# Kernel tuning notes

Measured on AMD Instinct MI355X. Metric: run time of the kernel, lower is better.

## Reference

```python
import jax, jax.numpy as jnp
import numpy as np

EPS = 1e-6

def _ln(x, g, b):
    mu = jnp.mean(x, axis=-1, keepdims=True)
    var = jnp.mean(jnp.square(x - mu), axis=-1, keepdims=True)
    return (x - mu) * jax.lax.rsqrt(var + EPS) * g + b

def setup_inputs() -> dict:
    key = jax.random.key(0)
    ks = jax.random.split(key, 8)
    B, T, D = 4, 4096, 1024
    H = 16
    Dff = 4 * D
    s = 1.0 / np.sqrt(D)
    sf = 1.0 / np.sqrt(Dff)
    return {
        "x": jax.random.normal(ks[0], (B, T, D), dtype=jnp.float32),
        "wq": jax.random.uniform(ks[1], (D, D), jnp.float32, -s, s),
        "wk": jax.random.uniform(ks[2], (D, D), jnp.float32, -s, s),
        "wv": jax.random.uniform(ks[3], (D, D), jnp.float32, -s, s),
        "wo": jax.random.uniform(ks[4], (D, D), jnp.float32, -s, s),
        "ln1_g": jnp.ones((D,), jnp.float32),
        "ln1_b": jnp.zeros((D,), jnp.float32),
        "w1": jax.random.uniform(ks[5], (D, Dff), jnp.float32, -s, s),
        "b1": jnp.zeros((Dff,), jnp.float32),
        "w2": jax.random.uniform(ks[6], (Dff, D), jnp.float32, -sf, sf),
        "b2": jnp.zeros((D,), jnp.float32),
        "ln2_g": jnp.ones((D,), jnp.float32),
        "ln2_b": jnp.zeros((D,), jnp.float32),
    }

def reference(x, wq, wk, wv, wo, ln1_g, ln1_b, w1, b1, w2, b2, ln2_g, ln2_b):
    B, T, D = x.shape
    H = 16
    dk = D // H
    x1 = _ln(x, ln1_g, ln1_b)
    q = (x1 @ wq).reshape(B, T, H, dk)
    k = (x1 @ wk).reshape(B, T, H, dk)
    v = (x1 @ wv).reshape(B, T, H, dk)
    # NOTE: faithful to source -- attention mixes HEADS at each token position
    # attn[b,t,h,g] = softmax_g( sum_d q[b,t,h,d]*k[b,t,g,d] / sqrt(dk) )
    attn = jax.nn.softmax(jnp.einsum('bthd,btgd->bthg', q / np.sqrt(dk), k), axis=-1)
    o = jnp.einsum('bthg,btgd->bthd', attn, v)
    # faithful head-major reshape: transpose(1,2).contiguous().view(B,T,-1)
    o = jnp.transpose(o, (0, 2, 1, 3)).reshape(B, T, H * dk)
    o = o @ wo
    q2 = _ln(o + x, ln1_g, ln1_b)  # same layer_norm params reused
    h = jax.nn.gelu(q2 @ w1 + b1, approximate=False)
    y = h @ w2 + b2 + q2
    return _ln(y, ln2_g, ln2_b)
```

## Files before the change

### kernel.cpp

```cpp
#include <hip/hip_runtime.h>


typedef __attribute__((ext_vector_type(8))) short s16x8;
typedef __attribute__((ext_vector_type(4))) short s16x4;
typedef __attribute__((ext_vector_type(4))) float f32x4;

__device__ __forceinline__ short f2bf(float x) {
  unsigned u = __builtin_bit_cast(unsigned, x);
  u = (u + 0x7FFFu + ((u >> 16) & 1u)) >> 16;
  return (short)u;
}
__device__ __forceinline__ float bf2f(short s) {
  unsigned u = ((unsigned)(unsigned short)s) << 16;
  return __builtin_bit_cast(float, u);
}

__device__ __forceinline__ void ld_g2l16(const short* g, const short* l) {
  __builtin_amdgcn_global_load_lds(
      (const __attribute__((address_space(1))) void*)g,
      (__attribute__((address_space(3))) void*)l, 16, 0, 0);
}

__device__ __forceinline__ s16x8 lds_read8(const short* smem, int off) {
  const __attribute__((address_space(3))) short* p =
      (const __attribute__((address_space(3))) short*)smem;
  return *(const __attribute__((address_space(3))) s16x8*)(p + off);
}
__device__ __forceinline__ void lds_wr_f32(const short* smem, int foff,
                                           float v) {
  __attribute__((address_space(3))) float* p =
      (__attribute__((address_space(3))) float*)smem;
  p[foff] = v;
}
__device__ __forceinline__ float lds_rd_f32(const short* smem, int foff) {
  const __attribute__((address_space(3))) float* p =
      (const __attribute__((address_space(3))) float*)smem;
  return p[foff];
}

__device__ __forceinline__ float fast_gelu(float v) {
  float y = 0.7978845608f * (v + 0.044715f * v * v * v);
  float ay = fabsf(y);
  float t = __expf(-2.0f * ay);
  float th = (1.0f - t) * __frcp_rn(1.0f + t);
  th = (y >= 0.f) ? th : -th;
  return 0.5f * v * (1.0f + th);
}

#define MFMA16(va, vb, vc) \
  __builtin_amdgcn_mfma_f32_16x16x32_bf16(va, vb, vc, 0, 0, 0)

template <int EPI>
__device__ __forceinline__ void epi_chunk(
    const short* smem, int two, int lane, const f32x4* accm ,
    void* __restrict__ outp, const float* __restrict__ bias, int N, int rowb,
    int nb) {
  const int cc16 = lane & 15, hq = lane >> 4;
#pragma unroll
  for (int n = 0; n < 4; ++n)
#pragma unroll
    for (int r = 0; r < 4; ++r)
      lds_wr_f32(smem, two + (n * 16 + cc16) * 17 + hq * 4 + r, accm[n][r]);
  asm volatile("s_waitcnt lgkmcnt(0)" ::: "memory");
  if constexpr (EPI == 0 || EPI == 2) {
    const int grp = lane & 7;
#pragma unroll
    for (int p = 0; p < 2; ++p) {
      const int row = p * 8 + (lane >> 3);
      const int colb = grp * 8;
      s16x8 ov;
#pragma unroll
      for (int i = 0; i < 8; ++i) {
        float v = lds_rd_f32(smem, two + (colb + i) * 17 + row);
        if constexpr (EPI == 2) v = fast_gelu(v + bias[nb + colb + i]);
        ov[i] = f2bf(v);
      }
      *(s16x8*)((short*)outp + (size_t)(rowb + row) * N + nb + colb) = ov;
    }
  } else {
    const int seg = lane & 3;
    const int row = lane >> 2;
#pragma unroll
    for (int k = 0; k < 4; ++k) {
      const int colb = seg * 4 + k * 16;
      float4 v4;
      v4.x = lds_rd_f32(smem, two + (colb + 0) * 17 + row);
      v4.y = lds_rd_f32(smem, two + (colb + 1) * 17 + row);
      v4.z = lds_rd_f32(smem, two + (colb + 2) * 17 + row);
      v4.w = lds_rd_f32(smem, two + (colb + 3) * 17 + row);
      float* gp = (float*)outp + (size_t)(rowb + row) * N + nb + colb;
      if constexpr (EPI == 4) {
        float4 pv = *(const float4*)gp;
        v4.x += pv.x; v4.y += pv.y; v4.z += pv.z; v4.w += pv.w;
        if (bias) {
          v4.x += bias[nb + colb + 0];
          v4.y += bias[nb + colb + 1];
          v4.z += bias[nb + colb + 2];
          v4.w += bias[nb + colb + 3];
        }
      }
      *(float4*)gp = v4;
    }
  }
  asm volatile("s_waitcnt lgkmcnt(0)" ::: "memory");
}

template <int EPI>
__global__ __launch_bounds__(512, 2) void gemm256(
    const short* __restrict__ A, const short* __restrict__ BT,
    void* __restrict__ outp, const float* __restrict__ bias, int N, int K) {
  extern __shared__ __align__(16) short smem[];

  const int t = threadIdx.x;
  const int lane = t & 63, w = t >> 6;
  const int wm = w >> 2, wn = w & 3;

  const int nbn = N >> 8;
  const int oi = (int)blockIdx.x;
  const int seq = oi >> 3;
  const int bq = seq / nbn;
  const int bm = (oi & 7) * 8 + bq;
  const int bn = seq - bq * nbn;

  const int l8 = lane >> 3;
  const int lcw = ((lane & 7) ^ l8) * 8;
  const short* gA = A + (size_t)(bm * 256 + w * 8 + l8) * K + lcw;
  const short* gB = BT + (size_t)(bn * 256 + w * 8 + l8) * K + lcw;
  const int lb = w * 512;

  auto stage = [&](const short* g, int bufo, int h, int kt) {
    const int go = h * 128 * K + kt * 64;
    ld_g2l16(g + go, smem + bufo + h * 8192 + lb);
    ld_g2l16(g + go + 64 * K, smem + bufo + h * 8192 + 4096 + lb);
  };

  const int fr = lane & 15, fc = lane >> 4;
  const int baseA = (wm * 128 + fr) * 64;
  const int baseB = (wn * 64 + fr) * 64;
  const int sl0 = (fc ^ (fr & 7)) * 8;
  const int sl1 = ((4 + fc) ^ (fr & 7)) * 8;

  f32x4 acc[8][4];
#pragma unroll
  for (int m = 0; m < 8; ++m)
#pragma unroll
    for (int n = 0; n < 4; ++n) acc[m][n] = (f32x4){0.f, 0.f, 0.f, 0.f};

  const int nt = K >> 6;

  stage(gA, 0, 0, 0);
  stage(gA, 0, 1, 0);
  stage(gB, 32768, 0, 0);
  stage(gB, 32768, 1, 0);
  if (nt > 1) {
    stage(gA, 16384, 0, 1);
    stage(gA, 16384, 1, 1);
    stage(gB, 49152, 0, 1);
    stage(gB, 49152, 1, 1);
    asm volatile("s_waitcnt vmcnt(8)" ::: "memory");
  } else {
    asm volatile("s_waitcnt vmcnt(0)" ::: "memory");
  }
  __builtin_amdgcn_s_barrier();
  asm volatile("" ::: "memory");

  for (int u = 0; u < nt; ++u) {
    const bool pf = (u + 2 < nt);
    const int pa = (u & 1) << 14;
    const int pb = 32768 + pa;

    s16x8 a0[4][2], a1[4][2], b0[2][2], b1[2][2];
#pragma unroll
    for (int mi = 0; mi < 4; ++mi) {
      a0[mi][0] = lds_read8(smem, pa + baseA + mi * 1024 + sl0);
      a0[mi][1] = lds_read8(smem, pa + baseA + mi * 1024 + sl1);
    }
#pragma unroll
    for (int ni = 0; ni < 2; ++ni) {
      b0[ni][0] = lds_read8(smem, pb + baseB + ni * 1024 + sl0);
      b0[ni][1] = lds_read8(smem, pb + baseB + ni * 1024 + sl1);
    }
#pragma unroll
    for (int ni = 0; ni < 2; ++ni) {
      b1[ni][0] = lds_read8(smem, pb + baseB + 2048 + ni * 1024 + sl0);
      b1[ni][1] = lds_read8(smem, pb + baseB + 2048 + ni * 1024 + sl1);
    }
#pragma unroll
    for (int mi = 0; mi < 4; ++mi) {
      a1[mi][0] = lds_read8(smem, pa + baseA + 4096 + mi * 1024 + sl0);
      a1[mi][1] = lds_read8(smem, pa + baseA + 4096 + mi * 1024 + sl1);
    }

    __builtin_amdgcn_s_setprio(1);
#pragma unroll
    for (int mi = 0; mi < 4; ++mi)
#pragma unroll
      for (int ni = 0; ni < 2; ++ni) {
        acc[mi][ni] = MFMA16(a0[mi][0], b0[ni][0], acc[mi][ni]);
        acc[mi][ni] = MFMA16(a0[mi][1], b0[ni][1], acc[mi][ni]);
      }
#pragma unroll
    for (int mi = 0; mi < 4; ++mi)
#pragma unroll
      for (int ni = 0; ni < 2; ++ni) {
        acc[mi][2 + ni] = MFMA16(a0[mi][0], b1[ni][0], acc[mi][2 + ni]);
        acc[mi][2 + ni] = MFMA16(a0[mi][1], b1[ni][1], acc[mi][2 + ni]);
      }
#pragma unroll
    for (int mi = 0; mi < 4; ++mi)
#pragma unroll
      for (int ni = 0; ni < 2; ++ni) {
        acc[4 + mi][2 + ni] = MFMA16(a1[mi][0], b1[ni][0], acc[4 + mi][2 + ni]);
        acc[4 + mi][2 + ni] = MFMA16(a1[mi][1], b1[ni][1], acc[4 + mi][2 + ni]);
      }
    __builtin_amdgcn_s_setprio(0);

    asm volatile("s_waitcnt lgkmcnt(0)" ::: "memory");
    __builtin_amdgcn_s_barrier();
    asm volatile("" ::: "memory");

    if (pf) {
      stage(gB, pb, 0, u + 2);
      stage(gB, pb, 1, u + 2);
      stage(gA, pa, 0, u + 2);
      stage(gA, pa, 1, u + 2);
    }

    __builtin_amdgcn_s_setprio(1);
#pragma unroll
    for (int mi = 0; mi < 4; ++mi)
#pragma unroll
      for (int ni = 0; ni < 2; ++ni) {
        acc[4 + mi][ni] = MFMA16(a1[mi][0], b0[ni][0], acc[4 + mi][ni]);
        acc[4 + mi][ni] = MFMA16(a1[mi][1], b0[ni][1], acc[4 + mi][ni]);
      }
    __builtin_amdgcn_s_setprio(0);

    if (pf) {
      asm volatile("s_waitcnt vmcnt(8)" ::: "memory");
    } else {
      asm volatile("s_waitcnt vmcnt(0)" ::: "memory");
    }
    __builtin_amdgcn_s_barrier();
    asm volatile("" ::: "memory");
  }

  const int two = w * 1088;
  const int mb = bm * 256 + wm * 128;
  const int nb = bn * 256 + wn * 64;
#pragma unroll
  for (int m = 0; m < 8; ++m)
    epi_chunk<EPI>(smem, two, lane, acc[m], outp, bias, N, mb + m * 16, nb);
}

template <int EPI>
__global__ __launch_bounds__(512, 4) void gemm128(
    const short* __restrict__ A, const short* __restrict__ BT,
    void* __restrict__ outp, const float* __restrict__ bias, int N, int K) {
  extern __shared__ __align__(16) short smem[];

  const int t = threadIdx.x;
  const int lane = t & 63, w = t >> 6;
  const int wm = w >> 2, wn = w & 3;

  const int nbn = N >> 8;
  const int oi = (int)blockIdx.x;
  const int seq = oi >> 3;
  const int bq = seq / nbn;
  const int bm = (oi & 7) * 16 + bq;
  const int bn = seq - bq * nbn;

  const int lr = lane >> 2;
  const int lc = ((lane & 3) - ((lane >> 3) & 3)) & 3;
  const short* gA = A + (size_t)(bm * 128 + lr) * K + lc * 8;
  const short* gB = BT + (size_t)(bn * 256 + lr) * K + lc * 8;

  auto stageT = [&](int par, int kt) {
    ld_g2l16(gA + (size_t)(w * 16) * K + kt * 32, smem + par + w * 512);
    ld_g2l16(gB + (size_t)(2 * w * 16) * K + kt * 32,
             smem + par + 4096 + 2 * w * 512);
    ld_g2l16(gB + (size_t)((2 * w + 1) * 16) * K + kt * 32,
             smem + par + 4096 + (2 * w + 1) * 512);
  };

  const int fr = lane & 15, fc = lane >> 4;
  const int sl = ((fc + (fr >> 1)) & 3) * 8;
  const int baseA = (wm * 64 + fr) * 32 + sl;
  const int baseB = 4096 + (wn * 64 + fr) * 32 + sl;

  f32x4 acc[4][4];
#pragma unroll
  for (int m = 0; m < 4; ++m)
#pragma unroll
    for (int n = 0; n < 4; ++n) acc[m][n] = (f32x4){0.f, 0.f, 0.f, 0.f};

  const int nt = K >> 5;

  stageT(0, 0);
  stageT(12288, 1);
  asm volatile("s_waitcnt vmcnt(3)" ::: "memory");
  __builtin_amdgcn_s_barrier();
  asm volatile("" ::: "memory");

  int pcur = 0, pnxt = 12288, pprv = 24576;
  for (int u = 0; u < nt; ++u) {
    const bool pf = (u + 2 < nt);

    if (pf) stageT(pprv, u + 2);

    s16x8 a[4], b[4];
#pragma unroll
    for (int i = 0; i < 4; ++i)
      a[i] = lds_read8(smem, pcur + baseA + i * 512);
#pragma unroll
    for (int i = 0; i < 4; ++i)
      b[i] = lds_read8(smem, pcur + baseB + i * 512);

    __builtin_amdgcn_s_setprio(1);
#pragma unroll
    for (int mi = 0; mi < 4; ++mi)
#pragma unroll
      for (int ni = 0; ni < 4; ++ni)
        acc[mi][ni] = MFMA16(a[mi], b[ni], acc[mi][ni]);
    __builtin_amdgcn_s_setprio(0);

    asm volatile("s_waitcnt lgkmcnt(0)" ::: "memory");
    if (pf) {
      asm volatile("s_waitcnt vmcnt(3)" ::: "memory");
    } else {
      asm volatile("s_waitcnt vmcnt(0)" ::: "memory");
    }
    __builtin_amdgcn_s_barrier();
    asm volatile("" ::: "memory");

    const int tmp = pcur;
    pcur = pnxt;
    pnxt = pprv;
    pprv = tmp;
  }

  const int two = w * 1088;
  const int mb = bm * 128 + wm * 64;
  const int nb = bn * 256 + wn * 64;
#pragma unroll
  for (int m = 0; m < 4; ++m)
    epi_chunk<EPI>(smem, two, lane, acc[m], outp, bias, N, mb + m * 16, nb);
}

__global__ __launch_bounds__(256) void ln_k(
    const float* __restrict__ in, const float* __restrict__ add,
    const float* __restrict__ g, const float* __restrict__ b,
    float* __restrict__ outf, short* __restrict__ outb) {
  const int row = blockIdx.x;
  const size_t off = (size_t)row * 1024;
  const int t = threadIdx.x;
  float4 v = ((const float4*)(in + off))[t];
  if (add) {
    float4 w = ((const float4*)(add + off))[t];
    v.x += w.x; v.y += w.y; v.z += w.z; v.w += w.w;
  }
  float s = v.x + v.y + v.z + v.w;
  float ss = v.x * v.x + v.y * v.y + v.z * v.z + v.w * v.w;
#pragma unroll
  for (int o = 32; o > 0; o >>= 1) {
    s += __shfl_xor(s, o, 64);
    ss += __shfl_xor(ss, o, 64);
  }
  __shared__ float ps[4], pss[4];
  const int lane = t & 63, wave = t >> 6;
  if (lane == 0) { ps[wave] = s; pss[wave] = ss; }
  __syncthreads();
  s = ps[0] + ps[1] + ps[2] + ps[3];
  ss = pss[0] + pss[1] + pss[2] + pss[3];
  const float mean = s * (1.0f / 1024.0f);
  const float var = ss * (1.0f / 1024.0f) - mean * mean;
  const float rstd = rsqrtf(var + 1e-6f);
  const float4 gv = ((const float4*)g)[t];
  const float4 bv = ((const float4*)b)[t];
  float4 o4;
  o4.x = (v.x - mean) * rstd * gv.x + bv.x;
  o4.y = (v.y - mean) * rstd * gv.y + bv.y;
  o4.z = (v.z - mean) * rstd * gv.z + bv.z;
  o4.w = (v.w - mean) * rstd * gv.w + bv.w;
  if (outf) ((float4*)(outf + off))[t] = o4;
  if (outb) {
    s16x4 ob;
    ob[0] = f2bf(o4.x); ob[1] = f2bf(o4.y);
    ob[2] = f2bf(o4.z); ob[3] = f2bf(o4.w);
    *(s16x4*)(outb + off + t * 4) = ob;
  }
}

__device__ __forceinline__ void wconv_tile(const float* __restrict__ W,
                                           short* __restrict__ WT, int K,
                                           int N, int n0, int k0,
                                           float (*tile)[33], int c, int r) {
#pragma unroll
  for (int rr = r; rr < 32; rr += 8)
    tile[rr][c] = W[(size_t)(k0 + rr) * N + n0 + c];
  __syncthreads();
#pragma unroll
  for (int rr = r; rr < 32; rr += 8)
    WT[(size_t)(n0 + rr) * K + k0 + c] = f2bf(tile[c][rr]);
}

__global__ __launch_bounds__(256) void wconv_all(
    const float* __restrict__ wq, const float* __restrict__ wk,
    const float* __restrict__ wv, const float* __restrict__ wo,
    const float* __restrict__ w1, const float* __restrict__ w2,
    short* __restrict__ WQKVT, short* __restrict__ WOT,
    short* __restrict__ W1T, short* __restrict__ W2aT,
    short* __restrict__ W2bT) {
  __shared__ float tile[32][33];
  const int t = threadIdx.x;
  const int c = t & 31, r = t >> 5;
  const int i = blockIdx.x;
  if (i < 4096) {
    const int seg = i >> 10, j = i & 1023;
    const int n0 = (j & 31) * 32, k0 = (j >> 5) * 32;
    const float* src = (seg == 0) ? wq : (seg == 1) ? wk : (seg == 2) ? wv : wo;
    short* dst = (seg == 3) ? WOT : WQKVT + (size_t)seg * 1024 * 1024;
    wconv_tile(src, dst, 1024, 1024, n0, k0, tile, c, r);
  } else if (i < 8192) {
    const int j = i - 4096;
    const int n0 = (j & 127) * 32, k0 = (j >> 7) * 32;
    wconv_tile(w1, W1T, 1024, 4096, n0, k0, tile, c, r);
  } else if (i < 10240) {
    const int j = i - 8192;
    const int n0 = (j & 31) * 32, k0 = (j >> 5) * 32;
    wconv_tile(w2, W2aT, 2048, 1024, n0, k0, tile, c, r);
  } else {
    const int j = i - 10240;
    const int n0 = (j & 31) * 32, k0 = (j >> 5) * 32;
    wconv_tile(w2 + (size_t)2048 * 1024, W2bT, 2048, 1024, n0, k0, tile, c, r);
  }
}

__global__ __launch_bounds__(256) void attn_k(const short* __restrict__ qkv,
                                              short* __restrict__ omix) {
  __shared__ float Qs[4][16][65];
  __shared__ float Ks[4][16][65];
  __shared__ float Vs[4][16][65];
  __shared__ float Ps[4][16][17];
  const int lane = threadIdx.x & 63;
  const int wave = threadIdx.x >> 6;
  const int tok = blockIdx.x * 4 + wave;
  const short* base = qkv + (size_t)tok * 3072;

#pragma unroll
  for (int half = 0; half < 2; half++) {
    const int e = half * 512 + lane * 8;
    const int h = e >> 6, d = e & 63;
    s16x8 rq = *(const s16x8*)(base + e);
    s16x8 rk = *(const s16x8*)(base + 1024 + e);
    s16x8 rv = *(const s16x8*)(base + 2048 + e);
#pragma unroll
    for (int j = 0; j < 8; j++) {
      Qs[wave][h][d + j] = bf2f(rq[j]);
      Ks[wave][h][d + j] = bf2f(rk[j]);
      Vs[wave][h][d + j] = bf2f(rv[j]);
    }
  }
  __syncthreads();

  const int h = lane & 15;
  const int g0 = (lane >> 4) * 4;
  float sc[4] = {0.f, 0.f, 0.f, 0.f};
  for (int d = 0; d < 64; d++) {
    const float qv = Qs[wave][h][d];
#pragma unroll
    for (int i = 0; i < 4; i++) sc[i] += qv * Ks[wave][g0 + i][d];
  }
#pragma unroll
  for (int i = 0; i < 4; i++) sc[i] *= 0.125f;
  float m = fmaxf(fmaxf(sc[0], sc[1]), fmaxf(sc[2], sc[3]));
  m = fmaxf(m, __shfl_xor(m, 16, 64));
  m = fmaxf(m, __shfl_xor(m, 32, 64));
  float e[4], sum = 0.f;
#pragma unroll
  for (int i = 0; i < 4; i++) { e[i] = __expf(sc[i] - m); sum += e[i]; }
  sum += __shfl_xor(sum, 16, 64);
  sum += __shfl_xor(sum, 32, 64);
  const float inv = __frcp_rn(sum);
#pragma unroll
  for (int i = 0; i < 4; i++) Ps[wave][h][g0 + i] = e[i] * inv;
  __syncthreads();

  const int d0 = (lane >> 4) * 16;
  float o[16];
#pragma unroll
  for (int dd = 0; dd < 16; dd++) o[dd] = 0.f;
  for (int gg = 0; gg < 16; gg++) {
    const float pv = Ps[wave][h][gg];
#pragma unroll
    for (int dd = 0; dd < 16; dd++) o[dd] += pv * Vs[wave][gg][d0 + dd];
  }

  const int b = tok >> 12, t = tok & 4095;
  const size_t dst =
      ((size_t)(b * 4096 + h * 256 + (t >> 4))) * 1024 + (t & 15) * 64 + d0;
  s16x8 w0, w1;
#pragma unroll
  for (int j = 0; j < 8; j++) { w0[j] = f2bf(o[j]); w1[j] = f2bf(o[8 + j]); }
  *(s16x8*)(omix + dst) = w0;
  *(s16x8*)(omix + dst + 8) = w1;
}

extern "C" void kernel_launch(void* const* d_in, const int* in_sizes, int n_in,
                              void* d_out, int out_size, void* d_ws,
                              size_t ws_size, hipStream_t stream) {
  const float* x    = (const float*)d_in[0];
  const float* wq   = (const float*)d_in[1];
  const float* wk   = (const float*)d_in[2];
  const float* wv   = (const float*)d_in[3];
  const float* wo   = (const float*)d_in[4];
  const float* ln1g = (const float*)d_in[5];
  const float* ln1b = (const float*)d_in[6];
  const float* w1   = (const float*)d_in[7];
  const float* b1   = (const float*)d_in[8];
  const float* w2   = (const float*)d_in[9];
  const float* b2   = (const float*)d_in[10];
  const float* ln2g = (const float*)d_in[11];
  const float* ln2b = (const float*)d_in[12];
  float* out = (float*)d_out;

  char* ws = (char*)d_ws;
  const size_t MB = 1024ull * 1024ull;
  const size_t NEEDED = 152 * MB;
  if (ws_size < NEEDED) return;

  short* QKV  = (short*)(ws + 0);
  short* Q2B  = (short*)(ws + 0);
  short* Hbuf = (short*)(ws + 32 * MB);
  short* X1 = (short*)(ws + 96 * MB);
  short* WQKVT = (short*)(ws + 128 * MB);
  short* WOT   = (short*)(ws + 134 * MB);
  short* W1T   = (short*)(ws + 136 * MB);
  short* W2aT  = (short*)(ws + 144 * MB);
  short* W2bT  = (short*)(ws + 148 * MB);

  const dim3 B256(256);
  const dim3 B512(512);
  const unsigned LDS256 = 131072;
  const unsigned LDS128 = 73728;

  static bool attr_done = false;
  if (!attr_done) {
    attr_done = true;
    void (*k0)(const short*, const short*, void*, const float*, int, int) =
        gemm256<0>;
    void (*k2)(const short*, const short*, void*, const float*, int, int) =
        gemm256<2>;
    (void)hipFuncSetAttribute((const void*)k0,
        hipFuncAttributeMaxDynamicSharedMemorySize, (int)LDS256);
    (void)hipFuncSetAttribute((const void*)k2,
        hipFuncAttributeMaxDynamicSharedMemorySize, (int)LDS256);
    void (*h1)(const short*, const short*, void*, const float*, int, int) =
        gemm128<1>;
    void (*h4)(const short*, const short*, void*, const float*, int, int) =
        gemm128<4>;
    (void)hipFuncSetAttribute((const void*)h1,
        hipFuncAttributeMaxDynamicSharedMemorySize, (int)LDS128);
    (void)hipFuncSetAttribute((const void*)h4,
        hipFuncAttributeMaxDynamicSharedMemorySize, (int)LDS128);
  }

  wconv_all<<<dim3(12288), B256, 0, stream>>>(wq, wk, wv, wo, w1, w2, WQKVT,
                                              WOT, W1T, W2aT, W2bT);

  ln_k<<<16384, B256, 0, stream>>>(x, nullptr, ln1g, ln1b, nullptr, X1);

  gemm256<0><<<dim3(768), B512, LDS256, stream>>>(X1, WQKVT, QKV, nullptr,
                                                  3072, 1024);

  attn_k<<<4096, B256, 0, stream>>>(QKV, X1);

  gemm128<1><<<dim3(512), B512, LDS128, stream>>>(X1, WOT, out, nullptr,
                                                  1024, 1024);

  ln_k<<<16384, B256, 0, stream>>>(out, x, ln1g, ln1b, out, Q2B);

  gemm256<2><<<dim3(512), B512, LDS256, stream>>>(Q2B, W1T, Hbuf, b1,
                                                  2048, 1024);
  gemm128<4><<<dim3(512), B512, LDS128, stream>>>(Hbuf, W2aT, out, nullptr,
                                                  1024, 2048);

  gemm256<2><<<dim3(512), B512, LDS256, stream>>>(Q2B, W1T + 2048 * 1024,
                                                  Hbuf, b1 + 2048, 2048,
                                                  1024);
  gemm128<4><<<dim3(512), B512, LDS128, stream>>>(Hbuf, W2bT, out, b2,
                                                  1024, 2048);

  ln_k<<<16384, B256, 0, stream>>>(out, nullptr, ln2g, ln2b, out, nullptr);
}
```

Baseline: 772.3 us.

## Replace gemm128 with 256x128 tile, K=64 double-buffered GEMM for N=1024 projections

The 128x256 output-tile GEMM used for the Wo and W2 projections is replaced by a kernel with a 256x128 tile (8 waves laid out 4x2) and a K step of 64 instead of 32. It uses XOR-swizzled LDS rows and a two-stage buffer in place of the old three-stage ring. The prefetch for step u+2 is issued mid-iteration after a barrier, overlapping the last MFMA row with the global loads. The aim is fewer barriers per K and better issue overlap, at the cost of more LDS (96KB) and lower occupancy (launch bounds 2 instead of 4).

```diff
diff --git a/kernel.cpp b/kernel.cpp
--- a/kernel.cpp
+++ b/kernel.cpp
@@ -254,39 +254,46 @@
 }
 
 template <int EPI>
-__global__ __launch_bounds__(512, 4) void gemm128(
+__global__ __launch_bounds__(512, 2) void gemm192(
     const short* __restrict__ A, const short* __restrict__ BT,
     void* __restrict__ outp, const float* __restrict__ bias, int N, int K) {
   extern __shared__ __align__(16) short smem[];
 
   const int t = threadIdx.x;
   const int lane = t & 63, w = t >> 6;
-  const int wm = w >> 2, wn = w & 3;
-
-  const int nbn = N >> 8;
+  const int wm = w >> 1, wn = w & 1;
+
+  const int nbn = N >> 7;
   const int oi = (int)blockIdx.x;
   const int seq = oi >> 3;
   const int bq = seq / nbn;
-  const int bm = (oi & 7) * 16 + bq;
+  const int bm = (oi & 7) * 8 + bq;
   const int bn = seq - bq * nbn;
 
-  const int lr = lane >> 2;
-  const int lc = ((lane & 3) - ((lane >> 3) & 3)) & 3;
-  const short* gA = A + (size_t)(bm * 128 + lr) * K + lc * 8;
-  const short* gB = BT + (size_t)(bn * 256 + lr) * K + lc * 8;
-
-  auto stageT = [&](int par, int kt) {
-    ld_g2l16(gA + (size_t)(w * 16) * K + kt * 32, smem + par + w * 512);
-    ld_g2l16(gB + (size_t)(2 * w * 16) * K + kt * 32,
-             smem + par + 4096 + 2 * w * 512);
-    ld_g2l16(gB + (size_t)((2 * w + 1) * 16) * K + kt * 32,
-             smem + par + 4096 + (2 * w + 1) * 512);
+  const int l8 = lane >> 3;
+  const int lcw = ((lane & 7) ^ l8) * 8;
+  const short* gA = A + (size_t)(bm * 256 + w * 8 + l8) * K + lcw;
+  const short* gB = BT + (size_t)(bn * 128 + w * 8 + l8) * K + lcw;
+  const int lb = w * 512;
+
+  auto stageA = [&](int bufo, int kt) {
+    const int k64 = kt * 64;
+    ld_g2l16(gA + k64, smem + bufo + lb);
+    ld_g2l16(gA + 64 * K + k64, smem + bufo + 4096 + lb);
+    ld_g2l16(gA + 128 * K + k64, smem + bufo + 8192 + lb);
+    ld_g2l16(gA + 192 * K + k64, smem + bufo + 12288 + lb);
   };
+  auto stageB = [&](int bufo, int kt) {
+    const int k64 = kt * 64;
+    ld_g2l16(gB + k64, smem + bufo + lb);
+    ld_g2l16(gB + 64 * K + k64, smem + bufo + 4096 + lb);
+  };
 
   const int fr = lane & 15, fc = lane >> 4;
-  const int sl = ((fc + (fr >> 1)) & 3) * 8;
-  const int baseA = (wm * 64 + fr) * 32 + sl;
-  const int baseB = 4096 + (wn * 64 + fr) * 32 + sl;
+  const int baseA = (wm * 64 + fr) * 64;
+  const int baseB = (wn * 64 + fr) * 64;
+  const int sl0 = (fc ^ (fr & 7)) * 8;
+  const int sl1 = ((4 + fc) ^ (fr & 7)) * 8;
 
   f32x4 acc[4][4];
 #pragma unroll
@@ -294,54 +301,72 @@
 #pragma unroll
     for (int n = 0; n < 4; ++n) acc[m][n] = (f32x4){0.f, 0.f, 0.f, 0.f};
 
-  const int nt = K >> 5;
-
-  stageT(0, 0);
-  stageT(12288, 1);
-  asm volatile("s_waitcnt vmcnt(3)" ::: "memory");
+  const int nt = K >> 6;
+
+  stageA(0, 0);
+  stageB(32768, 0);
+  stageA(16384, 1);
+  stageB(40960, 1);
+  asm volatile("s_waitcnt vmcnt(6)" ::: "memory");
   __builtin_amdgcn_s_barrier();
   asm volatile("" ::: "memory");
 
-  int pcur = 0, pnxt = 12288, pprv = 24576;
   for (int u = 0; u < nt; ++u) {
     const bool pf = (u + 2 < nt);
-
-    if (pf) stageT(pprv, u + 2);
-
-    s16x8 a[4], b[4];
-#pragma unroll
-    for (int i = 0; i < 4; ++i)
-      a[i] = lds_read8(smem, pcur + baseA + i * 512);
-#pragma unroll
-    for (int i = 0; i < 4; ++i)
-      b[i] = lds_read8(smem, pcur + baseB + i * 512);
+    const int pa = (u & 1) << 14;
+    const int pb = 32768 + ((u & 1) << 13);
+
+    s16x8 a[4][2], b[4][2];
+#pragma unroll
+    for (int mi = 0; mi < 4; ++mi) {
+      a[mi][0] = lds_read8(smem, pa + baseA + mi * 1024 + sl0);
+      a[mi][1] = lds_read8(smem, pa + baseA + mi * 1024 + sl1);
+    }
+#pragma unroll
+    for (int ni = 0; ni < 4; ++ni) {
+      b[ni][0] = lds_read8(smem, pb + baseB + ni * 1024 + sl0);
+      b[ni][1] = lds_read8(smem, pb + baseB + ni * 1024 + sl1);
+    }
 
     __builtin_amdgcn_s_setprio(1);
 #pragma unroll
-    for (int mi = 0; mi < 4; ++mi)
-#pragma unroll
-      for (int ni = 0; ni < 4; ++ni)
-        acc[mi][ni] = MFMA16(a[mi], b[ni], acc[mi][ni]);
+    for (int mi = 0; mi < 3; ++mi)
+#pragma unroll
+      for (int ni = 0; ni < 4; ++ni) {
+        acc[mi][ni] = MFMA16(a[mi][0], b[ni][0], acc[mi][ni]);
+        acc[mi][ni] = MFMA16(a[mi][1], b[ni][1], acc[mi][ni]);
+      }
     __builtin_amdgcn_s_setprio(0);
 
     asm volatile("s_waitcnt lgkmcnt(0)" ::: "memory");
+    __builtin_amdgcn_s_barrier();
+    asm volatile("" ::: "memory");
+
     if (pf) {
-      asm volatile("s_waitcnt vmcnt(3)" ::: "memory");
+      stageA(pa, u + 2);
+      stageB(pb, u + 2);
+    }
+
+    __builtin_amdgcn_s_setprio(1);
+#pragma unroll
+    for (int ni = 0; ni < 4; ++ni) {
+      acc[3][ni] = MFMA16(a[3][0], b[ni][0], acc[3][ni]);
+      acc[3][ni] = MFMA16(a[3][1], b[ni][1], acc[3][ni]);
+    }
+    __builtin_amdgcn_s_setprio(0);
+
+    if (pf) {
+      asm volatile("s_waitcnt vmcnt(6)" ::: "memory");
     } else {
       asm volatile("s_waitcnt vmcnt(0)" ::: "memory");
     }
     __builtin_amdgcn_s_barrier();
     asm volatile("" ::: "memory");
-
-    const int tmp = pcur;
-    pcur = pnxt;
-    pnxt = pprv;
-    pprv = tmp;
   }
 
   const int two = w * 1088;
-  const int mb = bm * 128 + wm * 64;
-  const int nb = bn * 256 + wn * 64;
+  const int mb = bm * 256 + wm * 64;
+  const int nb = bn * 128 + wn * 64;
 #pragma unroll
   for (int m = 0; m < 4; ++m)
     epi_chunk<EPI>(smem, two, lane, acc[m], outp, bias, N, mb + m * 16, nb);
@@ -542,7 +567,7 @@
   const dim3 B256(256);
   const dim3 B512(512);
   const unsigned LDS256 = 131072;
-  const unsigned LDS128 = 73728;
+  const unsigned LDS192 = 98304;
 
   static bool attr_done = false;
   if (!attr_done) {
@@ -555,14 +580,14 @@
         hipFuncAttributeMaxDynamicSharedMemorySize, (int)LDS256);
     (void)hipFuncSetAttribute((const void*)k2,
         hipFuncAttributeMaxDynamicSharedMemorySize, (int)LDS256);
-    void (*h1)(const short*, const short*, void*, const float*, int, int) =
-        gemm128<1>;
-    void (*h4)(const short*, const short*, void*, const float*, int, int) =
-        gemm128<4>;
-    (void)hipFuncSetAttribute((const void*)h1,
-        hipFuncAttributeMaxDynamicSharedMemorySize, (int)LDS128);
-    (void)hipFuncSetAttribute((const void*)h4,
-        hipFuncAttributeMaxDynamicSharedMemorySize, (int)LDS128);
+    void (*g1)(const short*, const short*, void*, const float*, int, int) =
+        gemm192<1>;
+    void (*g4)(const short*, const short*, void*, const float*, int, int) =
+        gemm192<4>;
+    (void)hipFuncSetAttribute((const void*)g1,
+        hipFuncAttributeMaxDynamicSharedMemorySize, (int)LDS192);
+    (void)hipFuncSetAttribute((const void*)g4,
+        hipFuncAttributeMaxDynamicSharedMemorySize, (int)LDS192);
   }
 
   wconv_all<<<dim3(12288), B256, 0, stream>>>(wq, wk, wv, wo, w1, w2, WQKVT,
@@ -575,20 +600,20 @@
 
   attn_k<<<4096, B256, 0, stream>>>(QKV, X1);
 
-  gemm128<1><<<dim3(512), B512, LDS128, stream>>>(X1, WOT, out, nullptr,
+  gemm192<1><<<dim3(512), B512, LDS192, stream>>>(X1, WOT, out, nullptr,
                                                   1024, 1024);
 
   ln_k<<<16384, B256, 0, stream>>>(out, x, ln1g, ln1b, out, Q2B);
 
   gemm256<2><<<dim3(512), B512, LDS256, stream>>>(Q2B, W1T, Hbuf, b1,
                                                   2048, 1024);
-  gemm128<4><<<dim3(512), B512, LDS128, stream>>>(Hbuf, W2aT, out, nullptr,
+  gemm192<4><<<dim3(512), B512, LDS192, stream>>>(Hbuf, W2aT, out, nullptr,
                                                   1024, 2048);
 
   gemm256<2><<<dim3(512), B512, LDS256, stream>>>(Q2B, W1T + 2048 * 1024,
                                                   Hbuf, b1 + 2048, 2048,
                                                   1024);
-  gemm128<4><<<dim3(512), B512, LDS128, stream>>>(Hbuf, W2bT, out, b2,
+  gemm192<4><<<dim3(512), B512, LDS192, stream>>>(Hbuf, W2bT, out, b2,
                                                   1024, 2048);
 
   ln_k<<<16384, B256, 0, stream>>>(out, nullptr, ln2g, ln2b, out, nullptr);
```

Measured after the change: 770.7 us. About the same (-0.2%).
